# Performance work log

Measured on AMD Instinct MI355X. Metric: run time of the kernel, lower is better.

The kernel has to match this reference:

```python
import jax, jax.numpy as jnp
import numpy as np

B, M, FIN, FOUT = 8, 2048, 256, 128
ALPHA = 0.2  # LeakyReLU negative slope
NEG_INF = -9e15


def _xavier_uniform(key, shape, gain):
    fan_in, fan_out = shape[0], shape[1]
    bound = gain * np.sqrt(6.0 / (fan_in + fan_out))
    return jax.random.uniform(key, shape, jnp.float32, -bound, bound)


def setup_inputs() -> dict:
    key = jax.random.key(0)
    k1, k2, k3, k4 = jax.random.split(key, 4)
    x = jax.random.normal(k1, (B, M, FIN), jnp.float32)
    adj1 = jax.random.randint(k2, (B, M, M), 0, 2).astype(jnp.int32)
    W = _xavier_uniform(k3, (FIN, FOUT), gain=2.0)
    a = _xavier_uniform(k4, (2 * FOUT, 1), gain=2.0)
    return {"input": x, "adj1": adj1, "W": W, "a": a}


def reference(input, adj1, W, a):
    # h: [B, M, FOUT]
    h = jnp.matmul(input, W)
    # e[b,i,j] = leakyrelu( concat(h_i, h_j) . a ) = leakyrelu( h_i.a1 + h_j.a2 )
    a1 = a[:FOUT, 0]   # [FOUT]
    a2 = a[FOUT:, 0]   # [FOUT]
    f1 = jnp.einsum('bme,e->bm', h, a1)  # source (row i) term
    f2 = jnp.einsum('bme,e->bm', h, a2)  # target (col j) term
    e = jax.nn.leaky_relu(f1[:, :, None] + f2[:, None, :], negative_slope=ALPHA)  # [B,M,M]
    scores = jnp.where(adj1 > 0, e, NEG_INF)
    attention = jax.nn.softmax(scores, axis=-1)
    # dropout is identity in eval mode (training=False)
    h_prime = jnp.matmul(attention, h)  # [B,M,FOUT]
    return jax.nn.elu(h_prime)  # concat=True branch
```

## Files before the change

### kernel.cpp

```cpp
#include <hip/hip_runtime.h>
#include <math.h>

#define B_    8
#define M_    2048
#define FIN_  256
#define FOUT_ 128
#define ALPHA_ 0.2f
#define NEG_INF_ -9.0e15f

typedef unsigned short u16;
typedef __attribute__((ext_vector_type(8))) short bf16x8;
typedef __attribute__((ext_vector_type(4))) float f32x4;

static __device__ __forceinline__ u16 f2bf(float f) {
  union { float f; unsigned u; } v; v.f = f;
  unsigned r = v.u + 0x7FFFu + ((v.u >> 16) & 1u);
  return (u16)(r >> 16);
}

__global__ __launch_bounds__(256) void k_conv(const float* __restrict__ x,
                                              const float* __restrict__ W,
                                              u16* __restrict__ xbf,
                                              u16* __restrict__ Wt) {
  const int blk = blockIdx.x;
  if (blk < 2048) {
    const size_t base = ((size_t)blk * 256 + threadIdx.x) * 8;
    float4 v0 = *(const float4*)(x + base);
    float4 v1 = *(const float4*)(x + base + 4);
    union { u16 u[8]; uint4 q; } o;
    o.u[0] = f2bf(v0.x); o.u[1] = f2bf(v0.y); o.u[2] = f2bf(v0.z); o.u[3] = f2bf(v0.w);
    o.u[4] = f2bf(v1.x); o.u[5] = f2bf(v1.y); o.u[6] = f2bf(v1.z); o.u[7] = f2bf(v1.w);
    *(uint4*)(xbf + base) = o.q;
  } else {
    const int id = (blk - 2048) * 256 + threadIdx.x;
    const int f = id >> 8;
    const int k = id & 255;
    Wt[f * FIN_ + k] = f2bf(W[(size_t)k * FOUT_ + f]);
  }
}

__global__ __launch_bounds__(128) void k_xw(const u16* __restrict__ xbf,
                                            const u16* __restrict__ Wt,
                                            const float* __restrict__ a,
                                            u16* __restrict__ ht,
                                            float* __restrict__ f1,
                                            float* __restrict__ f2) {
  int blk = blockIdx.x;
  blk = (blk & 7) * 128 + (blk >> 3);
  const int b    = blk >> 7;
  const int row0 = (blk & 127) * 16;
  const int rowg = b * M_ + row0;
  const int tid  = threadIdx.x;
  const int w  = tid >> 6;
  const int l  = tid & 63;
  const int lr = l & 15;
  const int g  = l >> 4;
  const int fbase = w * 64;

  f32x4 acc[4];
#pragma unroll
  for (int ft = 0; ft < 4; ++ft) acc[ft] = (f32x4){0.f, 0.f, 0.f, 0.f};

  const u16* xr = xbf + (size_t)(rowg + lr) * FIN_;
#pragma unroll
  for (int ks = 0; ks < 8; ++ks) {
    bf16x8 af = *(const bf16x8*)(xr + ks * 32 + g * 8);
#pragma unroll
    for (int ft = 0; ft < 4; ++ft) {
      bf16x8 bf = *(const bf16x8*)(Wt + (fbase + ft * 16 + lr) * FIN_ + ks * 32 + g * 8);
      acc[ft] = __builtin_amdgcn_mfma_f32_16x16x32_bf16(af, bf, acc[ft], 0, 0, 0);
    }
  }

  __shared__ float sf1[2][16], sf2[2][16];
  float v1[4] = {0.f, 0.f, 0.f, 0.f};
  float v2[4] = {0.f, 0.f, 0.f, 0.f};
#pragma unroll
  for (int ft = 0; ft < 4; ++ft) {
    const float a1v = a[fbase + ft * 16 + lr];
    const float a2v = a[FOUT_ + fbase + ft * 16 + lr];
#pragma unroll
    for (int j = 0; j < 4; ++j) {
      v1[j] += acc[ft][j] * a1v;
      v2[j] += acc[ft][j] * a2v;
    }
  }
#pragma unroll
  for (int off = 1; off < 16; off <<= 1) {
#pragma unroll
    for (int j = 0; j < 4; ++j) {
      v1[j] += __shfl_xor(v1[j], off);
      v2[j] += __shfl_xor(v2[j], off);
    }
  }
  if (lr == 0) {
#pragma unroll
    for (int j = 0; j < 4; ++j) {
      sf1[w][g * 4 + j] = v1[j];
      sf2[w][g * 4 + j] = v2[j];
    }
  }

  __shared__ float hs[16][132];
#pragma unroll
  for (int ft = 0; ft < 4; ++ft)
#pragma unroll
    for (int j = 0; j < 4; ++j)
      hs[g * 4 + j][fbase + ft * 16 + lr] = acc[ft][j];
  __syncthreads();

  if (tid < 16) {
    f1[rowg + tid] = sf1[0][tid] + sf1[1][tid];
    f2[rowg + tid] = sf2[0][tid] + sf2[1][tid];
  }
  const int f = tid;
  union { u16 u[16]; uint4 q[2]; } hb;
#pragma unroll
  for (int i = 0; i < 16; ++i) hb.u[i] = f2bf(hs[i][f]);
  u16* dst = ht + (size_t)(b * FOUT_ + f) * M_ + row0;
  *(uint4*)(dst)     = hb.q[0];
  *(uint4*)(dst + 8) = hb.q[1];
}

__global__ __launch_bounds__(256) void k_attn(const u16* __restrict__ ht,
                                              const int* __restrict__ adj,
                                              const float* __restrict__ f1,
                                              const float* __restrict__ f2,
                                              float* __restrict__ out) {
  int blk = blockIdx.x;
  blk = (blk & 7) * 128 + (blk >> 3);
  const int b    = blk >> 7;
  const int row0 = (blk & 127) * 16;
  const int tid = threadIdx.x;
  const int w  = tid >> 6;
  const int l  = tid & 63;
  const int lr = l & 15;
  const int g  = l >> 4;
  const int r  = tid >> 4;
  const int ts = tid & 15;

  __shared__ __align__(16) u16 P[16][128];
  __shared__ float smx[16], ssum[16], sscale[16], f1s[16];

  if (tid < 16) {
    smx[tid]  = -INFINITY;
    ssum[tid] = 0.f;
    f1s[tid]  = f1[b * M_ + row0 + tid];
  }

  f32x4 acc0 = (f32x4){0.f, 0.f, 0.f, 0.f};
  f32x4 acc1 = (f32x4){0.f, 0.f, 0.f, 0.f};

  const int fbase = w * 32;
  const int* ap   = adj + ((size_t)b * M_ + row0 + r) * M_ + ts * 8;
  const float* fp = f2 + b * M_ + ts * 8;
  const u16* hp0  = ht + (size_t)(b * FOUT_ + fbase + lr) * M_ + g * 8;
  const u16* hp1  = hp0 + 16 * M_;
  char* Pb = (char*)P;

  int4   ajA = *(const int4*)(ap);
  int4   ajB = *(const int4*)(ap + 4);
  float4 fvA = *(const float4*)(fp);
  float4 fvB = *(const float4*)(fp + 4);

  __syncthreads();

  for (int n0 = 0; n0 < M_; n0 += 128) {
    const int   aj[8] = {ajA.x, ajA.y, ajA.z, ajA.w, ajB.x, ajB.y, ajB.z, ajB.w};
    const float fv[8] = {fvA.x, fvA.y, fvA.z, fvA.w, fvB.x, fvB.y, fvB.z, fvB.w};
    if (n0 + 128 < M_) {
      ajA = *(const int4*)(ap + n0 + 128);
      ajB = *(const int4*)(ap + n0 + 132);
      fvA = *(const float4*)(fp + n0 + 128);
      fvB = *(const float4*)(fp + n0 + 132);
    }
    const float f1r = f1s[r];
    float s[8];
#pragma unroll
    for (int i = 0; i < 8; ++i) {
      float z = f1r + fv[i];
      float e = z > 0.f ? z : ALPHA_ * z;
      s[i] = aj[i] > 0 ? e : NEG_INF_;
    }
    float cmax = s[0];
#pragma unroll
    for (int i = 1; i < 8; ++i) cmax = fmaxf(cmax, s[i]);
#pragma unroll
    for (int off = 1; off < 16; off <<= 1) cmax = fmaxf(cmax, __shfl_xor(cmax, off));
    const float m_old = smx[r];
    const float m_new = fmaxf(m_old, cmax);
    const float scl   = __expf(m_old - m_new);
    float psum = 0.f;
#pragma unroll
    for (int i = 0; i < 8; ++i) {
      float p = __expf(s[i] - m_new);
      s[i] = p;
      psum += p;
    }
#pragma unroll
    for (int off = 1; off < 16; off <<= 1) psum += __shfl_xor(psum, off);
    if (ts == 0) {
      smx[r]    = m_new;
      ssum[r]   = ssum[r] * scl + psum;
      sscale[r] = scl;
    }
    union { u16 u[8]; uint4 q; } pw;
#pragma unroll
    for (int i = 0; i < 8; ++i) pw.u[i] = f2bf(s[i]);
    *(uint4*)(Pb + r * 256 + ((ts ^ (r & 7)) << 4)) = pw.q;
    __syncthreads();

    f32x4 scv = { sscale[g * 4], sscale[g * 4 + 1], sscale[g * 4 + 2], sscale[g * 4 + 3] };
    acc0 *= scv;
    acc1 *= scv;
#pragma unroll
    for (int ks = 0; ks < 4; ++ks) {
      bf16x8 af = *(const bf16x8*)(Pb + lr * 256 + (((ks * 4 + g) ^ (lr & 7)) << 4));
      bf16x8 b0 = *(const bf16x8*)(hp0 + n0 + ks * 32);
      bf16x8 b1 = *(const bf16x8*)(hp1 + n0 + ks * 32);
      acc0 = __builtin_amdgcn_mfma_f32_16x16x32_bf16(af, b0, acc0, 0, 0, 0);
      acc1 = __builtin_amdgcn_mfma_f32_16x16x32_bf16(af, b1, acc1, 0, 0, 0);
    }
    __syncthreads();
  }

  f32x4 inv = { 1.f / ssum[g * 4], 1.f / ssum[g * 4 + 1],
                1.f / ssum[g * 4 + 2], 1.f / ssum[g * 4 + 3] };
#pragma unroll
  for (int j = 0; j < 4; ++j) {
    const size_t orow = ((size_t)b * M_ + row0 + g * 4 + j) * FOUT_;
    float t0 = acc0[j] * inv[j];
    float t1 = acc1[j] * inv[j];
    out[orow + fbase + lr]      = t0 > 0.f ? t0 : __expf(t0) - 1.f;
    out[orow + fbase + 16 + lr] = t1 > 0.f ? t1 : __expf(t1) - 1.f;
  }
}

extern "C" void kernel_launch(void* const* d_in, const int* in_sizes, int n_in,
                              void* d_out, int out_size, void* d_ws, size_t ws_size,
                              hipStream_t stream) {
  const float* x   = (const float*)d_in[0];
  const int*   adj = (const int*)d_in[1];
  const float* W   = (const float*)d_in[2];
  const float* a   = (const float*)d_in[3];
  float* out = (float*)d_out;

  char* ws = (char*)d_ws;
  u16*   Wt  = (u16*)ws;
  float* f1  = (float*)(ws + 65536);
  float* f2  = (float*)(ws + 131072);
  u16*   ht  = (u16*)(ws + 196608);
  u16*   xbf = (u16*)(ws + 196608 + 8388608);

  hipLaunchKernelGGL(k_conv, dim3(2176), dim3(256), 0, stream, x, W, xbf, Wt);
  hipLaunchKernelGGL(k_xw,   dim3(1024), dim3(128), 0, stream, xbf, Wt, a, ht, f1, f2);
  hipLaunchKernelGGL(k_attn, dim3(1024), dim3(256), 0, stream, ht, adj, f1, f2, out);
}
```

Baseline: 263.4 us.

## Fuse x bf16 conversion into XW GEMM and double-buffer attention loop

Removes the separate x-to-bf16 conversion pass by converting fp32 x on the fly inside the XW kernel, so the bf16 copy of x is no longer written to and read back from memory. The attention kernel now double-buffers the P tile and the per-row scale in shared memory and register-prefetches the next tile's h, adj and f2 values. This drops one __syncthreads per iteration and overlaps global loads with the MFMAs. The cost is higher register pressure from the two 8-entry vector buffers and a redundant prefetch on the last iteration.

```diff
diff --git a/kernel.cpp b/kernel.cpp
--- a/kernel.cpp
+++ b/kernel.cpp
@@ -18,28 +18,15 @@
   return (u16)(r >> 16);
 }
 
-__global__ __launch_bounds__(256) void k_conv(const float* __restrict__ x,
-                                              const float* __restrict__ W,
-                                              u16* __restrict__ xbf,
-                                              u16* __restrict__ Wt) {
-  const int blk = blockIdx.x;
-  if (blk < 2048) {
-    const size_t base = ((size_t)blk * 256 + threadIdx.x) * 8;
-    float4 v0 = *(const float4*)(x + base);
-    float4 v1 = *(const float4*)(x + base + 4);
-    union { u16 u[8]; uint4 q; } o;
-    o.u[0] = f2bf(v0.x); o.u[1] = f2bf(v0.y); o.u[2] = f2bf(v0.z); o.u[3] = f2bf(v0.w);
-    o.u[4] = f2bf(v1.x); o.u[5] = f2bf(v1.y); o.u[6] = f2bf(v1.z); o.u[7] = f2bf(v1.w);
-    *(uint4*)(xbf + base) = o.q;
-  } else {
-    const int id = (blk - 2048) * 256 + threadIdx.x;
-    const int f = id >> 8;
-    const int k = id & 255;
-    Wt[f * FIN_ + k] = f2bf(W[(size_t)k * FOUT_ + f]);
-  }
-}
-
-__global__ __launch_bounds__(128) void k_xw(const u16* __restrict__ xbf,
+__global__ __launch_bounds__(256) void k_wt(const float* __restrict__ W,
+                                            u16* __restrict__ Wt) {
+  const int id = blockIdx.x * 256 + threadIdx.x;
+  const int f = id >> 8;
+  const int k = id & 255;
+  Wt[f * FIN_ + k] = f2bf(W[(size_t)k * FOUT_ + f]);
+}
+
+__global__ __launch_bounds__(128) void k_xw(const float* __restrict__ x,
                                             const u16* __restrict__ Wt,
                                             const float* __restrict__ a,
                                             u16* __restrict__ ht,
@@ -61,10 +48,16 @@
 #pragma unroll
   for (int ft = 0; ft < 4; ++ft) acc[ft] = (f32x4){0.f, 0.f, 0.f, 0.f};
 
-  const u16* xr = xbf + (size_t)(rowg + lr) * FIN_;
+  const float* xr = x + (size_t)(rowg + lr) * FIN_;
 #pragma unroll
   for (int ks = 0; ks < 8; ++ks) {
-    bf16x8 af = *(const bf16x8*)(xr + ks * 32 + g * 8);
+    float4 xa = *(const float4*)(xr + ks * 32 + g * 8);
+    float4 xc = *(const float4*)(xr + ks * 32 + g * 8 + 4);
+    bf16x8 af;
+    af[0] = (short)f2bf(xa.x); af[1] = (short)f2bf(xa.y);
+    af[2] = (short)f2bf(xa.z); af[3] = (short)f2bf(xa.w);
+    af[4] = (short)f2bf(xc.x); af[5] = (short)f2bf(xc.y);
+    af[6] = (short)f2bf(xc.z); af[7] = (short)f2bf(xc.w);
 #pragma unroll
     for (int ft = 0; ft < 4; ++ft) {
       bf16x8 bf = *(const bf16x8*)(Wt + (fbase + ft * 16 + lr) * FIN_ + ks * 32 + g * 8);
@@ -139,8 +132,9 @@
   const int r  = tid >> 4;
   const int ts = tid & 15;
 
-  __shared__ __align__(16) u16 P[16][128];
-  __shared__ float smx[16], ssum[16], sscale[16], f1s[16];
+  __shared__ __align__(16) u16 P[2][16][128];
+  __shared__ float sscale[2][16];
+  __shared__ float smx[16], ssum[16], f1s[16];
 
   if (tid < 16) {
     smx[tid]  = -INFINITY;
@@ -162,18 +156,20 @@
   int4   ajB = *(const int4*)(ap + 4);
   float4 fvA = *(const float4*)(fp);
   float4 fvB = *(const float4*)(fp + 4);
+  bf16x8 vbuf0[8], vbuf1[8];
+#pragma unroll
+  for (int ks = 0; ks < 4; ++ks) {
+    vbuf0[ks]     = *(const bf16x8*)(hp0 + ks * 32);
+    vbuf0[4 + ks] = *(const bf16x8*)(hp1 + ks * 32);
+  }
 
   __syncthreads();
 
-  for (int n0 = 0; n0 < M_; n0 += 128) {
+  auto iter = [&](int it, bf16x8 (&vcur)[8], bf16x8 (&vnxt)[8]) {
+    const int n0 = it * 128;
+    const int bi = it & 1;
     const int   aj[8] = {ajA.x, ajA.y, ajA.z, ajA.w, ajB.x, ajB.y, ajB.z, ajB.w};
     const float fv[8] = {fvA.x, fvA.y, fvA.z, fvA.w, fvB.x, fvB.y, fvB.z, fvB.w};
-    if (n0 + 128 < M_) {
-      ajA = *(const int4*)(ap + n0 + 128);
-      ajB = *(const int4*)(ap + n0 + 132);
-      fvA = *(const float4*)(fp + n0 + 128);
-      fvB = *(const float4*)(fp + n0 + 132);
-    }
     const float f1r = f1s[r];
     float s[8];
 #pragma unroll
@@ -200,28 +196,43 @@
 #pragma unroll
     for (int off = 1; off < 16; off <<= 1) psum += __shfl_xor(psum, off);
     if (ts == 0) {
-      smx[r]    = m_new;
-      ssum[r]   = ssum[r] * scl + psum;
-      sscale[r] = scl;
+      smx[r]       = m_new;
+      ssum[r]      = ssum[r] * scl + psum;
+      sscale[bi][r] = scl;
     }
     union { u16 u[8]; uint4 q; } pw;
 #pragma unroll
     for (int i = 0; i < 8; ++i) pw.u[i] = f2bf(s[i]);
-    *(uint4*)(Pb + r * 256 + ((ts ^ (r & 7)) << 4)) = pw.q;
+    *(uint4*)(Pb + bi * 4096 + r * 256 + ((ts ^ (r & 7)) << 4)) = pw.q;
     __syncthreads();
 
-    f32x4 scv = { sscale[g * 4], sscale[g * 4 + 1], sscale[g * 4 + 2], sscale[g * 4 + 3] };
+    const int nn = (it + 1 < 16) ? (n0 + 128) : 0;
+    ajA = *(const int4*)(ap + nn);
+    ajB = *(const int4*)(ap + nn + 4);
+    fvA = *(const float4*)(fp + nn);
+    fvB = *(const float4*)(fp + nn + 4);
+#pragma unroll
+    for (int ks = 0; ks < 4; ++ks) {
+      vnxt[ks]     = *(const bf16x8*)(hp0 + nn + ks * 32);
+      vnxt[4 + ks] = *(const bf16x8*)(hp1 + nn + ks * 32);
+    }
+    f32x4 scv = { sscale[bi][g * 4],     sscale[bi][g * 4 + 1],
+                  sscale[bi][g * 4 + 2], sscale[bi][g * 4 + 3] };
     acc0 *= scv;
     acc1 *= scv;
 #pragma unroll
     for (int ks = 0; ks < 4; ++ks) {
-      bf16x8 af = *(const bf16x8*)(Pb + lr * 256 + (((ks * 4 + g) ^ (lr & 7)) << 4));
-      bf16x8 b0 = *(const bf16x8*)(hp0 + n0 + ks * 32);
-      bf16x8 b1 = *(const bf16x8*)(hp1 + n0 + ks * 32);
-      acc0 = __builtin_amdgcn_mfma_f32_16x16x32_bf16(af, b0, acc0, 0, 0, 0);
-      acc1 = __builtin_amdgcn_mfma_f32_16x16x32_bf16(af, b1, acc1, 0, 0, 0);
-    }
-    __syncthreads();
+      bf16x8 af = *(const bf16x8*)(Pb + bi * 4096 + lr * 256 +
+                                   (((ks * 4 + g) ^ (lr & 7)) << 4));
+      acc0 = __builtin_amdgcn_mfma_f32_16x16x32_bf16(af, vcur[ks],     acc0, 0, 0, 0);
+      acc1 = __builtin_amdgcn_mfma_f32_16x16x32_bf16(af, vcur[4 + ks], acc1, 0, 0, 0);
+    }
+  };
+
+#pragma unroll 1
+  for (int it = 0; it < 16; it += 2) {
+    iter(it,     vbuf0, vbuf1);
+    iter(it + 1, vbuf1, vbuf0);
   }
 
   f32x4 inv = { 1.f / ssum[g * 4], 1.f / ssum[g * 4 + 1],
@@ -246,13 +257,12 @@
   float* out = (float*)d_out;
 
   char* ws = (char*)d_ws;
-  u16*   Wt  = (u16*)ws;
-  float* f1  = (float*)(ws + 65536);
-  float* f2  = (float*)(ws + 131072);
-  u16*   ht  = (u16*)(ws + 196608);
-  u16*   xbf = (u16*)(ws + 196608 + 8388608);
-
-  hipLaunchKernelGGL(k_conv, dim3(2176), dim3(256), 0, stream, x, W, xbf, Wt);
-  hipLaunchKernelGGL(k_xw,   dim3(1024), dim3(128), 0, stream, xbf, Wt, a, ht, f1, f2);
+  u16*   Wt = (u16*)ws;
+  float* f1 = (float*)(ws + 65536);
+  float* f2 = (float*)(ws + 131072);
+  u16*   ht = (u16*)(ws + 196608);
+
+  hipLaunchKernelGGL(k_wt,   dim3(128),  dim3(256), 0, stream, W, Wt);
+  hipLaunchKernelGGL(k_xw,   dim3(1024), dim3(128), 0, stream, x, Wt, a, ht, f1, f2);
   hipLaunchKernelGGL(k_attn, dim3(1024), dim3(256), 0, stream, ht, adj, f1, f2, out);
 }
```

Result: no change. 259.3 us (-1.6%).
